# Performance work log

Hardware: AMD Instinct MI355X
Metric: run time of the kernel (lower is better)

Reference implementation:

```python
import jax, jax.numpy as jnp
import numpy as np
import math

B, S, H, NH, FF = 4, 2048, 1024, 16, 4096
HD = H // NH  # head dim = 64

def gelu_tanh(x):
    # BERT/GPT tanh-approx gelu, matching the torch source
    return 0.5 * x * (1.0 + jnp.tanh(jnp.sqrt(2.0 / jnp.pi) * (x + 0.044715 * x * x * x)))

def layernorm(x, g, b, eps=1e-12):
    mu = jnp.mean(x, axis=-1, keepdims=True)
    var = jnp.mean(jnp.square(x - mu), axis=-1, keepdims=True)
    return (x - mu) * jax.lax.rsqrt(var + eps) * g + b

def setup_inputs() -> dict:
    key = jax.random.key(0)
    ks = jax.random.split(key, 16)
    std = 0.02
    d = {
        'x': jax.random.normal(ks[0], (B, S, H), jnp.float32),
        'attention_mask': jnp.zeros((B, 1, 1, S), jnp.float32),
        'Wq': jax.random.normal(ks[1], (H, H), jnp.float32) * std,
        'bq': jnp.zeros((H,), jnp.float32),
        'Wk': jax.random.normal(ks[2], (H, H), jnp.float32) * std,
        'bk': jnp.zeros((H,), jnp.float32),
        'Wv': jax.random.normal(ks[3], (H, H), jnp.float32) * std,
        'bv': jnp.zeros((H,), jnp.float32),
        'Wo': jax.random.normal(ks[4], (H, H), jnp.float32) * std,
        'bo': jnp.zeros((H,), jnp.float32),
        'ln1_g': jnp.ones((H,), jnp.float32),
        'ln1_b': jnp.zeros((H,), jnp.float32),
        'W1': jax.random.normal(ks[5], (H, FF), jnp.float32) * std,
        'b1': jnp.zeros((FF,), jnp.float32),
        'W2': jax.random.normal(ks[6], (FF, H), jnp.float32) * std,
        'b2': jnp.zeros((H,), jnp.float32),
        'ln2_g': jnp.ones((H,), jnp.float32),
        'ln2_b': jnp.zeros((H,), jnp.float32),
    }
    return d

def reference(x, attention_mask, Wq, bq, Wk, bk, Wv, bv, Wo, bo,
              ln1_g, ln1_b, W1, b1, W2, b2, ln2_g, ln2_b):
    # --- attention ---
    q = (x @ Wq + bq).reshape(B, S, NH, HD).transpose(0, 2, 1, 3)  # [B,NH,S,HD]
    k = (x @ Wk + bk).reshape(B, S, NH, HD).transpose(0, 2, 1, 3)
    v = (x @ Wv + bv).reshape(B, S, NH, HD).transpose(0, 2, 1, 3)
    scores = jnp.einsum('bhqd,bhkd->bhqk', q, k) / math.sqrt(HD)
    scores = scores + attention_mask
    probs = jax.nn.softmax(scores, axis=-1)  # dropout p=0 (eval)
    ctx = jnp.einsum('bhqk,bhkd->bhqd', probs, v)
    ctx = ctx.transpose(0, 2, 1, 3).reshape(B, S, H)
    attn_out = ctx @ Wo + bo
    # residual + LN (post-LN)
    x1 = layernorm(x + attn_out, ln1_g, ln1_b)
    # --- FFN ---
    ff = gelu_tanh(x1 @ W1 + b1) @ W2 + b2
    out = layernorm(x1 + ff, ln2_g, ln2_b)
    return out
```

## Files before the change

### kernel.cpp

```cpp
#include <hip/hip_runtime.h>

#define B_ 4
#define S_ 2048
#define H_ 1024
#define NH_ 16
#define HD_ 64
#define FF_ 4096

typedef __attribute__((ext_vector_type(8))) short bfx8;
typedef __attribute__((ext_vector_type(4))) float f32x4;
typedef __attribute__((ext_vector_type(16))) float f32x16;
typedef __attribute__((ext_vector_type(4))) unsigned short us4;

__device__ __forceinline__ unsigned short f2bf(float x) {
  union { float f; unsigned u; } c; c.f = x;
  unsigned r = c.u + 0x7FFFu + ((c.u >> 16) & 1u);
  return (unsigned short)(r >> 16);
}
__device__ __forceinline__ unsigned cvtpk(float a, float b) {
  unsigned r;
  asm("v_cvt_pk_bf16_f32 %0, %1, %2" : "=v"(r) : "v"(a), "v"(b));
  return r;
}
__device__ __forceinline__ f32x4 mfma16(bfx8 a, bfx8 b, f32x4 c) {
  return __builtin_amdgcn_mfma_f32_16x16x32_bf16(a, b, c, 0, 0, 0);
}
__device__ __forceinline__ f32x16 mfma32(bfx8 a, bfx8 b, f32x16 c) {
  return __builtin_amdgcn_mfma_f32_32x32x16_bf16(a, b, c, 0, 0, 0);
}
__device__ __forceinline__ void async16(const unsigned short* g, unsigned short* l) {
  __builtin_amdgcn_global_load_lds(
      (const __attribute__((address_space(1))) unsigned int*)g,
      (__attribute__((address_space(3))) unsigned int*)l, 16, 0, 0);
}
__device__ __forceinline__ float gelu_f(float x) {
  float u = 0.7978845608028654f * (x + 0.044715f * x * x * x);
  float e = __expf(2.f * u);
  float t = 1.f - 2.f / (e + 1.f);
  return 0.5f * x * (1.f + t);
}

__global__ __launch_bounds__(256) void k_cvt(const float* __restrict__ in,
                                             unsigned short* __restrict__ out, int n4) {
  int i = blockIdx.x * 256 + threadIdx.x;
  if (i >= n4) return;
  float4 v = ((const float4*)in)[i];
  us4 o; o.x = f2bf(v.x); o.y = f2bf(v.y); o.z = f2bf(v.z); o.w = f2bf(v.w);
  ((us4*)out)[i] = o;
}

__global__ __launch_bounds__(256) void k_cat3(const float* __restrict__ a,
                                              const float* __restrict__ b,
                                              const float* __restrict__ c,
                                              float* __restrict__ o) {
  int i = blockIdx.x * 256 + threadIdx.x;
  if (i >= 3 * H_) return;
  o[i] = i < H_ ? a[i] : (i < 2 * H_ ? b[i - H_] : c[i - 2 * H_]);
}

__global__ __launch_bounds__(256) void k_wtrans(const float* __restrict__ W,
                                                unsigned short* __restrict__ WT,
                                                int K, int N) {
  __shared__ float tile[64][65];
  int k0 = blockIdx.x * 64, n0 = blockIdx.y * 64;
  int t = threadIdx.x;
#pragma unroll
  for (int i = 0; i < 16; i++) {
    int li = t + i * 256;
    int kl = li >> 6, nl = li & 63;
    tile[kl][nl] = W[(size_t)(k0 + kl) * N + n0 + nl];
  }
  __syncthreads();
#pragma unroll
  for (int i = 0; i < 16; i++) {
    int li = t + i * 256;
    int nl = li >> 6, kl = li & 63;
    WT[(size_t)(n0 + nl) * K + k0 + kl] = f2bf(tile[kl][nl]);
  }
}

__global__ __launch_bounds__(256) void k_vtrans(const unsigned short* __restrict__ v,
                                                int ld, unsigned short* __restrict__ vt) {
  __shared__ unsigned short tile[64][65];
  int s0 = blockIdx.x * 64;
  int bh = blockIdx.y;
  int b = bh >> 4, h = bh & 15;
  int t = threadIdx.x;
#pragma unroll
  for (int i = 0; i < 16; i++) {
    int li = t + i * 256;
    int sl = li >> 6, dl = li & 63;
    tile[sl][dl] = v[(size_t)(b * S_ + s0 + sl) * ld + h * HD_ + dl];
  }
  __syncthreads();
#pragma unroll
  for (int i = 0; i < 16; i++) {
    int li = t + i * 256;
    int dl = li >> 6, sl = li & 63;
    vt[((size_t)bh * HD_ + dl) * S_ + s0 + sl] = tile[sl][dl];
  }
}

template <int EPI>
__global__ __launch_bounds__(256) void k_gemm_bt(
    const unsigned short* __restrict__ A, const unsigned short* __restrict__ BT,
    const float* __restrict__ bias, float* __restrict__ Cf,
    unsigned short* __restrict__ Cb, int M, int N, int K) {
  __shared__ unsigned short As[128 * 32];
  __shared__ unsigned short Bs[128 * 32];
  const int tid = threadIdx.x;
  const int bx = blockIdx.x, by = blockIdx.y;
  const int wid = tid >> 6, lane = tid & 63;
  const int wr = wid >> 1, wc = wid & 1;
  const int lrow = lane & 15, lk = lane >> 4;

  f32x4 acc[4][4] = {};

  const int arow = tid >> 2, aseg = tid & 3;
  const unsigned short* gA = A + (size_t)(by * 128 + arow) * K + aseg * 8;
  const unsigned short* gB = BT + (size_t)(bx * 128 + arow) * K + aseg * 8;
  unsigned short* lA0 = &As[(tid & ~63) * 8];
  unsigned short* lA1 = lA0 + 2048;
  unsigned short* lB0 = &Bs[(tid & ~63) * 8];
  unsigned short* lB1 = lB0 + 2048;

  for (int k0 = 0; k0 < K; k0 += 32) {
    async16(gA + k0, lA0);
    async16(gA + (size_t)64 * K + k0, lA1);
    async16(gB + k0, lB0);
    async16(gB + (size_t)64 * K + k0, lB1);
    __syncthreads();
    bfx8 af[4], bf[4];
#pragma unroll
    for (int m = 0; m < 4; m++)
      af[m] = *(const bfx8*)&As[(wr * 64 + m * 16 + lrow) * 32 + lk * 8];
#pragma unroll
    for (int n = 0; n < 4; n++)
      bf[n] = *(const bfx8*)&Bs[(wc * 64 + n * 16 + lrow) * 32 + lk * 8];
#pragma unroll
    for (int m = 0; m < 4; m++)
#pragma unroll
      for (int n = 0; n < 4; n++)
        acc[m][n] = mfma16(af[m], bf[n], acc[m][n]);
    __syncthreads();
  }

#pragma unroll
  for (int n = 0; n < 4; n++) {
    const int gcol = bx * 128 + wc * 64 + n * 16 + lrow;
    const float bz = bias[gcol];
#pragma unroll
    for (int m = 0; m < 4; m++) {
      const int gr = by * 128 + wr * 64 + m * 16 + lk * 4;
#pragma unroll
      for (int r = 0; r < 4; r++) {
        float v = acc[m][n][r] + bz;
        if (EPI == 3) v = gelu_f(v);
        size_t idx = (size_t)(gr + r) * N + gcol;
        if (EPI == 2) Cf[idx] = v;
        else Cb[idx] = f2bf(v);
      }
    }
  }
}

__global__ __launch_bounds__(256) void k_attn(
    const unsigned short* __restrict__ qkv, const unsigned short* __restrict__ vt,
    const float* __restrict__ mask, unsigned short* __restrict__ ctx) {
  __shared__ unsigned short lds[2][8192];
  const int id = blockIdx.x;
  const int jj = (id & 7) * 128 + (id >> 3);
  const int bh = jj >> 4, qb = jj & 15;
  const int b = bh >> 4, h = bh & 15;
  const int tid = threadIdx.x, wid = tid >> 6, lane = tid & 63;
  const int lq = lane & 31, hi = lane >> 5;
  const int q0 = qb * 128 + wid * 32;
  const int LD = 3 * H_;
  const int NT = S_ / 64;

  const size_t KC = ((size_t)b * S_ + (tid & 31)) * LD + H_ + h * HD_ +
                    (tid >> 6) * 16 + ((tid >> 5) & 1) * 8;
  const size_t VC = ((size_t)bh * HD_ + ((tid >> 6) & 1) * 32 + (tid & 31)) * S_ +
                    (tid >> 7) * 16 + ((tid >> 5) & 1) * 8;

  const size_t qrow = ((size_t)b * S_ + q0 + lq) * LD + h * HD_;
  bfx8 qf[4];
#pragma unroll
  for (int c = 0; c < 4; c++) qf[c] = *(const bfx8*)&qkv[qrow + c * 16 + hi * 8];

  {
    unsigned short* lb = &lds[0][wid * 512];
    async16(qkv + KC, lb);
    async16(qkv + KC + (size_t)32 * LD, lb + 2048);
    async16(vt + VC, lb + 4096);
    async16(vt + VC + 32, lb + 6144);
  }
  asm volatile("s_waitcnt vmcnt(0)" ::: "memory");
  __syncthreads();

  float m_run = -1e30f, l_run = 0.f;
  f32x16 o0 = {}, o1 = {};
  const float* mrow = mask + (size_t)b * S_;

  for (int t = 0; t < NT; t++) {
    const int bb = t & 1;
    if (t + 1 < NT) {
      unsigned short* lb = &lds[bb ^ 1][wid * 512];
      const size_t ko = KC + (size_t)((t + 1) * 64) * LD;
      const size_t vo = VC + (size_t)(t + 1) * 64;
      async16(qkv + ko, lb);
      async16(qkv + ko + (size_t)32 * LD, lb + 2048);
      async16(vt + vo, lb + 4096);
      async16(vt + vo + 32, lb + 6144);
    }
    const unsigned short* L = lds[bb];

    bfx8 kf0[4], kf1[4];
#pragma unroll
    for (int c = 0; c < 4; c++) {
      kf0[c] = *(const bfx8*)&L[(c * 64 + lane) * 8];
      kf1[c] = *(const bfx8*)&L[((4 + c) * 64 + lane) * 8];
    }
    f32x16 s0 = {}, s1 = {};
    __builtin_amdgcn_s_setprio(1);
#pragma unroll
    for (int c = 0; c < 4; c++) s0 = mfma32(kf0[c], qf[c], s0);
#pragma unroll
    for (int c = 0; c < 4; c++) s1 = mfma32(kf1[c], qf[c], s1);
    __builtin_amdgcn_s_setprio(0);

    const int kb = t * 64;
#pragma unroll
    for (int g = 0; g < 4; g++) {
      const f32x4 m0 = *(const f32x4*)&mrow[kb + g * 8 + hi * 4];
      const f32x4 m1 = *(const f32x4*)&mrow[kb + 32 + g * 8 + hi * 4];
#pragma unroll
      for (int i = 0; i < 4; i++) {
        s0[g * 4 + i] = s0[g * 4 + i] * 0.125f + m0[i];
        s1[g * 4 + i] = s1[g * 4 + i] * 0.125f + m1[i];
      }
    }
    float mx = s0[0];
#pragma unroll
    for (int r = 1; r < 16; r++) mx = fmaxf(mx, s0[r]);
#pragma unroll
    for (int r = 0; r < 16; r++) mx = fmaxf(mx, s1[r]);
    mx = fmaxf(mx, __shfl_xor(mx, 32));
    if (!__all(mx <= m_run + 8.f)) {
      const float m_new = fmaxf(m_run, mx);
      const float scale = __expf(m_run - m_new);
      l_run *= scale;
#pragma unroll
      for (int r = 0; r < 16; r++) { o0[r] *= scale; o1[r] *= scale; }
      m_run = m_new;
    }
    float ps = 0.f;
#pragma unroll
    for (int r = 0; r < 16; r++) { s0[r] = __expf(s0[r] - m_run); ps += s0[r]; }
#pragma unroll
    for (int r = 0; r < 16; r++) { s1[r] = __expf(s1[r] - m_run); ps += s1[r]; }
    ps += __shfl_xor(ps, 32);
    l_run += ps;

    unsigned t0A0 = cvtpk(s0[0], s0[1]), t0A1 = cvtpk(s0[2], s0[3]);
    unsigned t0B0 = cvtpk(s0[4], s0[5]), t0B1 = cvtpk(s0[6], s0[7]);
    unsigned t0C0 = cvtpk(s0[8], s0[9]), t0C1 = cvtpk(s0[10], s0[11]);
    unsigned t0D0 = cvtpk(s0[12], s0[13]), t0D1 = cvtpk(s0[14], s0[15]);
    unsigned t1A0 = cvtpk(s1[0], s1[1]), t1A1 = cvtpk(s1[2], s1[3]);
    unsigned t1B0 = cvtpk(s1[4], s1[5]), t1B1 = cvtpk(s1[6], s1[7]);
    unsigned t1C0 = cvtpk(s1[8], s1[9]), t1C1 = cvtpk(s1[10], s1[11]);
    unsigned t1D0 = cvtpk(s1[12], s1[13]), t1D1 = cvtpk(s1[14], s1[15]);
    unsigned x0 = __shfl_xor(hi ? t0A0 : t0B0, 32);
    unsigned x1 = __shfl_xor(hi ? t0A1 : t0B1, 32);
    unsigned x2 = __shfl_xor(hi ? t0C0 : t0D0, 32);
    unsigned x3 = __shfl_xor(hi ? t0C1 : t0D1, 32);
    unsigned x4 = __shfl_xor(hi ? t1A0 : t1B0, 32);
    unsigned x5 = __shfl_xor(hi ? t1A1 : t1B1, 32);
    unsigned x6 = __shfl_xor(hi ? t1C0 : t1D0, 32);
    unsigned x7 = __shfl_xor(hi ? t1C1 : t1D1, 32);
    union { unsigned u[4]; bfx8 v; } p00, p01, p10, p11;
    p00.u[0] = hi ? x0 : t0A0;  p00.u[1] = hi ? x1 : t0A1;
    p00.u[2] = hi ? t0B0 : x0;  p00.u[3] = hi ? t0B1 : x1;
    p01.u[0] = hi ? x2 : t0C0;  p01.u[1] = hi ? x3 : t0C1;
    p01.u[2] = hi ? t0D0 : x2;  p01.u[3] = hi ? t0D1 : x3;
    p10.u[0] = hi ? x4 : t1A0;  p10.u[1] = hi ? x5 : t1A1;
    p10.u[2] = hi ? t1B0 : x4;  p10.u[3] = hi ? t1B1 : x5;
    p11.u[0] = hi ? x6 : t1C0;  p11.u[1] = hi ? x7 : t1C1;
    p11.u[2] = hi ? t1D0 : x6;  p11.u[3] = hi ? t1D1 : x7;

    bfx8 v00 = *(const bfx8*)&L[4096 + (0 * 64 + lane) * 8];
    bfx8 v10 = *(const bfx8*)&L[4096 + (1 * 64 + lane) * 8];
    bfx8 v01 = *(const bfx8*)&L[4096 + (2 * 64 + lane) * 8];
    bfx8 v11 = *(const bfx8*)&L[4096 + (3 * 64 + lane) * 8];
    bfx8 v02 = *(const bfx8*)&L[4096 + (4 * 64 + lane) * 8];
    bfx8 v12 = *(const bfx8*)&L[4096 + (5 * 64 + lane) * 8];
    bfx8 v03 = *(const bfx8*)&L[4096 + (6 * 64 + lane) * 8];
    bfx8 v13 = *(const bfx8*)&L[4096 + (7 * 64 + lane) * 8];
    __builtin_amdgcn_s_setprio(1);
    o0 = mfma32(v00, p00.v, o0);
    o0 = mfma32(v01, p01.v, o0);
    o0 = mfma32(v02, p10.v, o0);
    o0 = mfma32(v03, p11.v, o0);
    o1 = mfma32(v10, p00.v, o1);
    o1 = mfma32(v11, p01.v, o1);
    o1 = mfma32(v12, p10.v, o1);
    o1 = mfma32(v13, p11.v, o1);
    __builtin_amdgcn_s_setprio(0);

    asm volatile("s_waitcnt vmcnt(0)" ::: "memory");
    __syncthreads();
  }

  const float inv = 1.f / l_run;
  unsigned short* crow = ctx + ((size_t)b * S_ + q0 + lq) * H_ + h * HD_;
#pragma unroll
  for (int g = 0; g < 4; g++) {
    us4 w0, w1;
#pragma unroll
    for (int i = 0; i < 4; i++) {
      w0[i] = f2bf(o0[g * 4 + i] * inv);
      w1[i] = f2bf(o1[g * 4 + i] * inv);
    }
    *(us4*)&crow[g * 8 + hi * 4] = w0;
    *(us4*)&crow[32 + g * 8 + hi * 4] = w1;
  }
}

template <int WB>
__global__ __launch_bounds__(256) void k_ln(
    const float* __restrict__ xa, const float* __restrict__ xb,
    const float* __restrict__ g, const float* __restrict__ bt,
    float* __restrict__ outf, unsigned short* __restrict__ outb) {
  const int row = blockIdx.x;
  const int t = threadIdx.x;
  const size_t off = (size_t)row * H_ + t * 4;
  float4 va = *(const float4*)(xa + off);
  float4 vb = *(const float4*)(xb + off);
  float v0 = va.x + vb.x, v1 = va.y + vb.y, v2 = va.z + vb.z, v3 = va.w + vb.w;
  float s = (v0 + v1) + (v2 + v3);
#pragma unroll
  for (int d = 1; d < 64; d <<= 1) s += __shfl_xor(s, d);
  __shared__ float red1[4], red2[4];
  const int wid = t >> 6, lane = t & 63;
  if (lane == 0) red1[wid] = s;
  __syncthreads();
  const float mean = (red1[0] + red1[1] + red1[2] + red1[3]) * (1.f / H_);
  float d0 = v0 - mean, d1 = v1 - mean, d2 = v2 - mean, d3 = v3 - mean;
  float ss = (d0 * d0 + d1 * d1) + (d2 * d2 + d3 * d3);
#pragma unroll
  for (int d = 1; d < 64; d <<= 1) ss += __shfl_xor(ss, d);
  if (lane == 0) red2[wid] = ss;
  __syncthreads();
  const float var = (red2[0] + red2[1] + red2[2] + red2[3]) * (1.f / H_);
  const float rstd = rsqrtf(var + 1e-12f);
  const float4 gv = *(const float4*)(g + t * 4);
  const float4 bv = *(const float4*)(bt + t * 4);
  float y0 = d0 * rstd * gv.x + bv.x;
  float y1 = d1 * rstd * gv.y + bv.y;
  float y2 = d2 * rstd * gv.z + bv.z;
  float y3 = d3 * rstd * gv.w + bv.w;
  float4 yo; yo.x = y0; yo.y = y1; yo.z = y2; yo.w = y3;
  *(float4*)(outf + off) = yo;
  if (WB) {
    us4 ob; ob.x = f2bf(y0); ob.y = f2bf(y1); ob.z = f2bf(y2); ob.w = f2bf(y3);
    *(us4*)(outb + off) = ob;
  }
}

extern "C" void kernel_launch(void* const* d_in, const int* in_sizes, int n_in,
                              void* d_out, int out_size, void* d_ws, size_t ws_size,
                              hipStream_t stream) {
  const float* x    = (const float*)d_in[0];
  const float* mask = (const float*)d_in[1];
  const float* Wq = (const float*)d_in[2];
  const float* bq = (const float*)d_in[3];
  const float* Wk = (const float*)d_in[4];
  const float* bk = (const float*)d_in[5];
  const float* Wv = (const float*)d_in[6];
  const float* bv = (const float*)d_in[7];
  const float* Wo = (const float*)d_in[8];
  const float* bo = (const float*)d_in[9];
  const float* g1  = (const float*)d_in[10];
  const float* be1 = (const float*)d_in[11];
  const float* W1 = (const float*)d_in[12];
  const float* b1 = (const float*)d_in[13];
  const float* W2 = (const float*)d_in[14];
  const float* b2 = (const float*)d_in[15];
  const float* g2  = (const float*)d_in[16];
  const float* be2 = (const float*)d_in[17];
  float* out = (float*)d_out;

  char* ws = (char*)d_ws;
  unsigned short* WT   = (unsigned short*)(ws + 0);
  unsigned short* XBF  = (unsigned short*)(ws + 8388608);
  unsigned short* QKV  = (unsigned short*)(ws + 25165824);
  unsigned short* VT   = (unsigned short*)(ws + 75497472);
  unsigned short* FFBF = (unsigned short*)(ws + 92274688);
  unsigned short* CTX  = (unsigned short*)(ws + 159383552);
  float* BIAS3 = (float*)CTX;
  float* ATTN  = (float*)QKV;
  float* X1    = ATTN;
  unsigned short* X1BF = XBF;
  float* FF2   = (float*)(ws + 58720256);

  k_cvt<<<8192, 256, 0, stream>>>(x, XBF, (B_ * S_ * H_) / 4);
  k_cat3<<<12, 256, 0, stream>>>(bq, bk, bv, BIAS3);
  k_wtrans<<<dim3(16, 16), 256, 0, stream>>>(Wq, WT, H_, H_);
  k_wtrans<<<dim3(16, 16), 256, 0, stream>>>(Wk, WT + (size_t)1024 * H_, H_, H_);
  k_wtrans<<<dim3(16, 16), 256, 0, stream>>>(Wv, WT + (size_t)2048 * H_, H_, H_);
  k_gemm_bt<0><<<dim3(24, 64), 256, 0, stream>>>(XBF, WT, BIAS3, nullptr, QKV,
                                                 B_ * S_, 3 * H_, H_);
  k_vtrans<<<dim3(32, 64), 256, 0, stream>>>(QKV + 2048, 3 * H_, VT);
  k_attn<<<1024, 256, 0, stream>>>(QKV, VT, mask, CTX);
  k_wtrans<<<dim3(16, 16), 256, 0, stream>>>(Wo, WT, H_, H_);
  k_gemm_bt<2><<<dim3(8, 64), 256, 0, stream>>>(CTX, WT, bo, ATTN, nullptr,
                                                B_ * S_, H_, H_);
  k_ln<1><<<8192, 256, 0, stream>>>(x, ATTN, g1, be1, X1, X1BF);
  k_wtrans<<<dim3(16, 64), 256, 0, stream>>>(W1, WT, H_, FF_);
  k_gemm_bt<3><<<dim3(32, 64), 256, 0, stream>>>(X1BF, WT, b1, nullptr, FFBF,
                                                 B_ * S_, FF_, H_);
  k_wtrans<<<dim3(64, 16), 256, 0, stream>>>(W2, WT, FF_, H_);
  k_gemm_bt<2><<<dim3(8, 64), 256, 0, stream>>>(FFBF, WT, b2, FF2, nullptr,
                                                B_ * S_, H_, FF_);
  k_ln<0><<<8192, 256, 0, stream>>>(X1, FF2, g2, be2, out, nullptr);
}
```

Measured before the change: 675.9 us.

## Replace GEMM with 256-row tiled, double-buffered 512-thread kernel and swizzled grid

Replaces the 128x128 single-buffered GEMM with a 256xBN tile kernel using 512 threads, two LDS stages and async prefetch two K-steps ahead. It also remaps workgroup IDs so neighbouring blocks share operand tiles in cache, and raises wave priority around the MFMA block. The goal is more data reuse per loaded tile and to hide global-to-LDS latency that the old load-sync-compute loop exposed. In exchange it uses more LDS and registers per block, which may lower occupancy, and the prefetch-then-barrier ordering is harder to get right.

```diff
diff --git a/kernel.cpp b/kernel.cpp
--- a/kernel.cpp
+++ b/kernel.cpp
@@ -101,62 +101,95 @@
   }
 }
 
-template <int EPI>
-__global__ __launch_bounds__(256) void k_gemm_bt(
+template <int BN, int WM, int EPI>
+__global__ __launch_bounds__(512, 2) void k_gemm256(
     const unsigned short* __restrict__ A, const unsigned short* __restrict__ BT,
     const float* __restrict__ bias, float* __restrict__ Cf,
-    unsigned short* __restrict__ Cb, int M, int N, int K) {
-  __shared__ unsigned short As[128 * 32];
-  __shared__ unsigned short Bs[128 * 32];
-  const int tid = threadIdx.x;
-  const int bx = blockIdx.x, by = blockIdx.y;
-  const int wid = tid >> 6, lane = tid & 63;
-  const int wr = wid >> 1, wc = wid & 1;
+    unsigned short* __restrict__ Cb, int M, int N, int K, int nbx) {
+  constexpr int WN = 8 / WM;
+  constexpr int MR = 256 / WM / 16;
+  constexpr int NR = BN / WN / 16;
+  constexpr int NB = BN / 128;
+  __shared__ unsigned short smA[2][256 * 32];
+  __shared__ unsigned short smB[2][BN * 32];
+
+  const int nwg = gridDim.x;
+  const int o = blockIdx.x;
+  const int swz = (o & 7) * (nwg >> 3) + (o >> 3);
+  const int bx = swz % nbx, by = swz / nbx;
+
+  const int tid = threadIdx.x, lane = tid & 63, wid = tid >> 6;
+  const int wm = wid & (WM - 1), wn = wid / WM;
   const int lrow = lane & 15, lk = lane >> 4;
-
-  f32x4 acc[4][4] = {};
-
-  const int arow = tid >> 2, aseg = tid & 3;
-  const unsigned short* gA = A + (size_t)(by * 128 + arow) * K + aseg * 8;
-  const unsigned short* gB = BT + (size_t)(bx * 128 + arow) * K + aseg * 8;
-  unsigned short* lA0 = &As[(tid & ~63) * 8];
-  unsigned short* lA1 = lA0 + 2048;
-  unsigned short* lB0 = &Bs[(tid & ~63) * 8];
-  unsigned short* lB1 = lB0 + 2048;
-
-  for (int k0 = 0; k0 < K; k0 += 32) {
-    async16(gA + k0, lA0);
-    async16(gA + (size_t)64 * K + k0, lA1);
-    async16(gB + k0, lB0);
-    async16(gB + (size_t)64 * K + k0, lB1);
+  const int rowM = by * 256, rowN = bx * BN;
+  const int srow = tid >> 2, scol = (tid & 3) * 8;
+  const unsigned short* gA = A + (size_t)(rowM + srow) * K + scol;
+  const unsigned short* gB = BT + (size_t)(rowN + srow) * K + scol;
+
+  f32x4 acc[MR][NR] = {};
+  const int NK = K / 32;
+
+#pragma unroll
+  for (int j = 0; j < 2; j++)
+    async16(gA + (size_t)j * 128 * K, &smA[0][tid * 8 + j * 4096]);
+#pragma unroll
+  for (int j = 0; j < NB; j++)
+    async16(gB + (size_t)j * 128 * K, &smB[0][tid * 8 + j * 4096]);
+#pragma unroll
+  for (int j = 0; j < 2; j++)
+    async16(gA + 32 + (size_t)j * 128 * K, &smA[1][tid * 8 + j * 4096]);
+#pragma unroll
+  for (int j = 0; j < NB; j++)
+    async16(gB + 32 + (size_t)j * 128 * K, &smB[1][tid * 8 + j * 4096]);
+  __syncthreads();
+
+  for (int t = 0; t < NK; t++) {
+    const unsigned short* LA = smA[t & 1];
+    const unsigned short* LB = smB[t & 1];
+    bfx8 af[MR], bf[NR];
+#pragma unroll
+    for (int m = 0; m < MR; m++)
+      af[m] = *(const bfx8*)&LA[(wm * (MR * 16) + m * 16 + lrow) * 32 + lk * 8];
+#pragma unroll
+    for (int n = 0; n < NR; n++)
+      bf[n] = *(const bfx8*)&LB[(wn * (NR * 16) + n * 16 + lrow) * 32 + lk * 8];
+    __builtin_amdgcn_s_setprio(1);
+#pragma unroll
+    for (int m = 0; m < MR; m++)
+#pragma unroll
+      for (int n = 0; n < NR; n++)
+        acc[m][n] = mfma16(af[m], bf[n], acc[m][n]);
+    __builtin_amdgcn_s_setprio(0);
+
     __syncthreads();
-    bfx8 af[4], bf[4];
-#pragma unroll
-    for (int m = 0; m < 4; m++)
-      af[m] = *(const bfx8*)&As[(wr * 64 + m * 16 + lrow) * 32 + lk * 8];
-#pragma unroll
-    for (int n = 0; n < 4; n++)
-      bf[n] = *(const bfx8*)&Bs[(wc * 64 + n * 16 + lrow) * 32 + lk * 8];
-#pragma unroll
-    for (int m = 0; m < 4; m++)
-#pragma unroll
-      for (int n = 0; n < 4; n++)
-        acc[m][n] = mfma16(af[m], bf[n], acc[m][n]);
-    __syncthreads();
-  }
-
-#pragma unroll
-  for (int n = 0; n < 4; n++) {
-    const int gcol = bx * 128 + wc * 64 + n * 16 + lrow;
+
+    if (t + 2 < NK) {
+      const int k0 = (t + 2) * 32;
+      unsigned short* dA = &smA[t & 1][tid * 8];
+      unsigned short* dB = &smB[t & 1][tid * 8];
+#pragma unroll
+      for (int j = 0; j < 2; j++)
+        async16(gA + k0 + (size_t)j * 128 * K, dA + j * 4096);
+#pragma unroll
+      for (int j = 0; j < NB; j++)
+        async16(gB + k0 + (size_t)j * 128 * K, dB + j * 4096);
+    }
+    __builtin_amdgcn_s_barrier();
+    __builtin_amdgcn_sched_barrier(0);
+  }
+
+#pragma unroll
+  for (int n = 0; n < NR; n++) {
+    const int gcol = rowN + wn * (NR * 16) + n * 16 + lrow;
     const float bz = bias[gcol];
 #pragma unroll
-    for (int m = 0; m < 4; m++) {
-      const int gr = by * 128 + wr * 64 + m * 16 + lk * 4;
+    for (int m = 0; m < MR; m++) {
+      const int grow = rowM + wm * (MR * 16) + m * 16 + lk * 4;
 #pragma unroll
       for (int r = 0; r < 4; r++) {
         float v = acc[m][n][r] + bz;
         if (EPI == 3) v = gelu_f(v);
-        size_t idx = (size_t)(gr + r) * N + gcol;
+        size_t idx = (size_t)(grow + r) * N + gcol;
         if (EPI == 2) Cf[idx] = v;
         else Cb[idx] = f2bf(v);
       }
@@ -408,19 +441,19 @@
   k_wtrans<<<dim3(16, 16), 256, 0, stream>>>(Wq, WT, H_, H_);
   k_wtrans<<<dim3(16, 16), 256, 0, stream>>>(Wk, WT + (size_t)1024 * H_, H_, H_);
   k_wtrans<<<dim3(16, 16), 256, 0, stream>>>(Wv, WT + (size_t)2048 * H_, H_, H_);
-  k_gemm_bt<0><<<dim3(24, 64), 256, 0, stream>>>(XBF, WT, BIAS3, nullptr, QKV,
-                                                 B_ * S_, 3 * H_, H_);
+  k_gemm256<256, 2, 0><<<384, 512, 0, stream>>>(XBF, WT, BIAS3, nullptr, QKV,
+                                                B_ * S_, 3 * H_, H_, 12);
   k_vtrans<<<dim3(32, 64), 256, 0, stream>>>(QKV + 2048, 3 * H_, VT);
   k_attn<<<1024, 256, 0, stream>>>(QKV, VT, mask, CTX);
   k_wtrans<<<dim3(16, 16), 256, 0, stream>>>(Wo, WT, H_, H_);
-  k_gemm_bt<2><<<dim3(8, 64), 256, 0, stream>>>(CTX, WT, bo, ATTN, nullptr,
-                                                B_ * S_, H_, H_);
+  k_gemm256<128, 4, 2><<<256, 512, 0, stream>>>(CTX, WT, bo, ATTN, nullptr,
+                                                B_ * S_, H_, H_, 8);
   k_ln<1><<<8192, 256, 0, stream>>>(x, ATTN, g1, be1, X1, X1BF);
   k_wtrans<<<dim3(16, 64), 256, 0, stream>>>(W1, WT, H_, FF_);
-  k_gemm_bt<3><<<dim3(32, 64), 256, 0, stream>>>(X1BF, WT, b1, nullptr, FFBF,
-                                                 B_ * S_, FF_, H_);
+  k_gemm256<256, 2, 3><<<512, 512, 0, stream>>>(X1BF, WT, b1, nullptr, FFBF,
+                                                B_ * S_, FF_, H_, 16);
   k_wtrans<<<dim3(64, 16), 256, 0, stream>>>(W2, WT, FF_, H_);
-  k_gemm_bt<2><<<dim3(8, 64), 256, 0, stream>>>(FFBF, WT, b2, FF2, nullptr,
-                                                B_ * S_, H_, FF_);
+  k_gemm256<128, 4, 2><<<256, 512, 0, stream>>>(FFBF, WT, b2, FF2, nullptr,
+                                                B_ * S_, H_, FF_, 8);
   k_ln<0><<<8192, 256, 0, stream>>>(X1, FF2, g2, be2, out, nullptr);
 }
```

New measurement: 697.7 us. 1.03x slower.
